# Optimization experiments

Measured on AMD Instinct MI355X. Metric: run time of the kernel, lower is better.

## Reference

```python
import jax, jax.numpy as jnp
import numpy as np

VOCAB = 32000   # config['vocab_size']
D = 512         # embedding dim
H = 512         # config['VarDecoder']['gru']['out_dims']
B = 32          # batch_size = len(batch['var_tok_lens'])
T = 128         # max_len = max(batch['pre_var_tok_lens'])
TOPK = 5        # config['VarDecoder']['topk']
BOS = 1         # tokenizer.bos_token_id
ALPHA = 0.2     # tf.nn.leaky_relu default alpha


def setup_inputs() -> dict:
    key = jax.random.key(0)
    ks = jax.random.split(key, 7)
    s = jnp.float32(0.02)
    return {
        "E": jax.random.normal(ks[0], (VOCAB, D), jnp.float32) * s,      # embedding table
        "Wx": jax.random.normal(ks[1], (D, 3 * H), jnp.float32) * s,     # GRU input kernel [z|r|h]
        "U": jax.random.normal(ks[2], (H, 3 * H), jnp.float32) * s,      # GRU recurrent kernel [z|r|h]
        "b_i": jnp.zeros((3 * H,), jnp.float32),                          # GRU input bias (reset_after)
        "b_r": jnp.zeros((3 * H,), jnp.float32),                          # GRU recurrent bias (reset_after)
        "Wo": jax.random.normal(ks[3], (H, VOCAB), jnp.float32) * s,     # Dense kernel
        "bo": jnp.zeros((VOCAB,), jnp.float32),                           # Dense bias
        "context": jax.random.normal(ks[4], (B, H), jnp.float32),        # initial GRU state
        "rand_idx": jax.random.randint(ks[5], (T, B), 0, TOPK, jnp.int32),  # per-step uniform top-k pick
    }


def reference(E, Wx, U, b_i, b_r, Wo, bo, context, rand_idx):
    def step(carry, ridx):
        tok, h = carry                               # tok: [B] int32, h: [B, H]
        x = jax.nn.leaky_relu(E[tok], ALPHA)         # embedding + leaky_relu  [B, D]
        xg = x @ Wx + b_i                            # [B, 3H]
        hg = h @ U + b_r                             # [B, 3H] (keras reset_after=True)
        xz, xr, xh = jnp.split(xg, 3, axis=-1)
        hz, hr, hh = jnp.split(hg, 3, axis=-1)
        z = jax.nn.sigmoid(xz + hz)
        r = jax.nn.sigmoid(xr + hr)
        cand = jnp.tanh(xh + r * hh)
        h2 = z * h + (1.0 - z) * cand                # keras GRU update
        logits = h2 @ Wo + bo                        # [B, VOCAB]
        _, topk_idx = jax.lax.top_k(logits, TOPK)    # [B, TOPK]
        sel = jnp.take_along_axis(topk_idx, ridx[:, None], axis=1)[:, 0]  # random pick among top-k
        return (sel, h2), logits

    tok0 = jnp.full((B,), BOS, jnp.int32)
    (_, _), logits = jax.lax.scan(step, (tok0, context), rand_idx)
    return jnp.transpose(logits, (1, 0, 2))          # [B, T, VOCAB]
```

## Files before the change

kernel.cpp:

```cpp
#include <hip/hip_runtime.h>
#include <hip/hip_cooperative_groups.h>

namespace cg = cooperative_groups;

#define VOCAB   32000
#define DIM     512
#define HDIM    512
#define BATCH   32
#define TSTEPS  128
#define TOPKN   5
#define BOSTOK  1
#define ALPHA   0.2f
#define G3H     1536

#define NBLK    256
#define NTHR    256
#define GEMMBLK 250
#define CPB     128
#define KH      256
#define H2LD    (KH + 1)

struct alignas(16) SMem {
    float h2h[BATCH][H2LD];
    float sx[DIM];
    float dd[3][64];
    float mbv[4][BATCH][TOPKN];
    int   mbi[4][BATCH][TOPKN];
    float mrgv[4];
    int   mrgi[4];
    int   mrgt[4];
};

__device__ __forceinline__ bool better(float v1, int i1, float v2, int i2) {
    return (v1 > v2) || (v1 == v2 && i1 < i2);
}

__device__ __forceinline__ void ins5(float (&lv)[TOPKN], int (&li)[TOPKN], float v, int i) {
    if (better(v, i, lv[4], li[4])) {
        lv[4] = v; li[4] = i;
#pragma unroll
        for (int q = 4; q > 0; --q) {
            if (better(lv[q], li[q], lv[q - 1], li[q - 1])) {
                float tv = lv[q]; lv[q] = lv[q - 1]; lv[q - 1] = tv;
                int   ti = li[q]; li[q] = li[q - 1]; li[q - 1] = ti;
            }
        }
    }
}

__device__ __forceinline__ float dot256(const float* __restrict__ M, const float* sv,
                                        int c, int kb, float acc) {
    const float* p = M + (size_t)kb * G3H + c;
    float wa[32], wb[32];
#pragma unroll
    for (int u = 0; u < 32; ++u) wa[u] = p[(size_t)u * G3H];
    for (int k0 = 0; k0 < KH; k0 += 64) {
#pragma unroll
        for (int u = 0; u < 32; ++u) wb[u] = p[(size_t)(k0 + 32 + u) * G3H];
#pragma unroll
        for (int u = 0; u < 32; ++u) acc = fmaf(sv[k0 + u], wa[u], acc);
        if (k0 + 64 < KH) {
#pragma unroll
            for (int u = 0; u < 32; ++u) wa[u] = p[(size_t)(k0 + 64 + u) * G3H];
        }
#pragma unroll
        for (int u = 0; u < 32; ++u) acc = fmaf(sv[k0 + 32 + u], wb[u], acc);
    }
    return acc;
}

__device__ __forceinline__ void stage_half(SMem& s, const float* __restrict__ src,
                                           int kb, int tid) {
#pragma unroll
    for (int it = 0; it < 8; ++it) {
        const int i  = tid + it * NTHR;
        const int bb = i >> 6;
        const int k4 = i & 63;
        const float4 v = *(const float4*)(src + (size_t)bb * DIM + kb + k4 * 4);
        float* d = &s.h2h[bb][k4 * 4];
        d[0] = v.x; d[1] = v.y; d[2] = v.z; d[3] = v.w;
    }
}

__device__ __forceinline__ void loadg(float4 (&wv)[8], float (&av)[8][4],
                                      const float* __restrict__ wp, const SMem& s,
                                      int bg, int kb, int k0) {
#pragma unroll
    for (int u = 0; u < 8; ++u) {
        wv[u] = *(const float4*)(wp + (size_t)(kb + k0 + u) * VOCAB);
#pragma unroll
        for (int bi = 0; bi < 4; ++bi)
            av[u][bi] = s.h2h[bg * 4 + bi][k0 + u];
    }
}

__device__ __forceinline__ void fmacg(float (&acc)[4][4], const float4 (&wv)[8],
                                      const float (&av)[8][4]) {
#pragma unroll
    for (int u = 0; u < 8; ++u) {
#pragma unroll
        for (int bi = 0; bi < 4; ++bi) {
            const float a = av[u][bi];
            acc[bi][0] = fmaf(a, wv[u].x, acc[bi][0]);
            acc[bi][1] = fmaf(a, wv[u].y, acc[bi][1]);
            acc[bi][2] = fmaf(a, wv[u].z, acc[bi][2]);
            acc[bi][3] = fmaf(a, wv[u].w, acc[bi][3]);
        }
    }
}

__device__ __forceinline__ void prologue_hg(SMem& s, int j, int tid,
                                            const float* __restrict__ U,
                                            const float* __restrict__ b_r,
                                            const float* __restrict__ hsrc,
                                            float* __restrict__ hg) {
    const int g  = j * 192 + tid;
    const int bb = (tid < 192) ? (g / G3H) : 0;
    const int c  = (tid < 192) ? (g - bb * G3H) : 0;
    float hacc = (tid < 192) ? b_r[c] : 0.f;
    for (int half = 0; half < 2; ++half) {
        const int kb = half * KH;
        __syncthreads();
        stage_half(s, hsrc, kb, tid);
        __syncthreads();
        if (tid < 192) hacc = dot256(U, s.h2h[bb], c, kb, hacc);
    }
    if (tid < 192) hg[g] = hacc;
}

__device__ __forceinline__ void phaseA(SMem& s, int j, int tid, int t,
    const float* __restrict__ U,  const float* __restrict__ b_r,
    const float* __restrict__ Wo, const float* __restrict__ bo,
    const float* __restrict__ hsrc, float* __restrict__ out,
    float* __restrict__ hg, float* __restrict__ pval, int* __restrict__ pidx)
{
    const int w   = tid >> 6;
    const int l   = tid & 63;
    const int bg  = l >> 3;
    const int cg2 = l & 7;
    const int cbase = j * CPB + w * 32 + cg2 * 4;
    const bool gemmer = (j < GEMMBLK);

    const int g     = j * 192 + tid;
    const int hb_bb = (tid < 192) ? (g / G3H) : 0;
    const int hb_c  = (tid < 192) ? (g - hb_bb * G3H) : 0;
    float hacc = (tid < 192) ? b_r[hb_c] : 0.f;

    float acc[4][4] = {};

    for (int half = 0; half < 2; ++half) {
        const int kb = half * KH;
        __syncthreads();
        stage_half(s, hsrc, kb, tid);
        __syncthreads();
        if (gemmer) {
            const float* wp = Wo + cbase;
            float4 wva[8], wvb[8];
            float  ava[8][4], avb[8][4];
            loadg(wva, ava, wp, s, bg, kb, 0);
            for (int k0 = 0; k0 < KH; k0 += 16) {
                loadg(wvb, avb, wp, s, bg, kb, k0 + 8);
                fmacg(acc, wva, ava);
                if (k0 + 16 < KH) loadg(wva, ava, wp, s, bg, kb, k0 + 16);
                fmacg(acc, wvb, avb);
            }
        }
        if (tid < 192) hacc = dot256(U, s.h2h[hb_bb], hb_c, kb, hacc);
    }

    if (tid < 192) hg[g] = hacc;

    if (gemmer) {
        const float4 bov = *(const float4*)(bo + cbase);
#pragma unroll
        for (int bi = 0; bi < 4; ++bi) {
            const int bb = bg * 4 + bi;
            float4 v;
            v.x = acc[bi][0] + bov.x;
            v.y = acc[bi][1] + bov.y;
            v.z = acc[bi][2] + bov.z;
            v.w = acc[bi][3] + bov.w;
            *(float4*)(out + ((size_t)bb * TSTEPS + t) * VOCAB + cbase) = v;

            float lv[TOPKN]; int li[TOPKN];
#pragma unroll
            for (int q = 0; q < TOPKN; ++q) { lv[q] = -INFINITY; li[q] = 0x7fffffff; }
            ins5(lv, li, v.x, cbase + 0);
            ins5(lv, li, v.y, cbase + 1);
            ins5(lv, li, v.z, cbase + 2);
            ins5(lv, li, v.w, cbase + 3);
#pragma unroll
            for (int mask = 1; mask < 8; mask <<= 1) {
                float ov[TOPKN]; int oi[TOPKN];
#pragma unroll
                for (int q = 0; q < TOPKN; ++q) {
                    ov[q] = __shfl_xor(lv[q], mask);
                    oi[q] = __shfl_xor(li[q], mask);
                }
#pragma unroll
                for (int q = 0; q < TOPKN; ++q) ins5(lv, li, ov[q], oi[q]);
            }
            if (cg2 == 0) {
#pragma unroll
                for (int q = 0; q < TOPKN; ++q) { s.mbv[w][bb][q] = lv[q]; s.mbi[w][bb][q] = li[q]; }
            }
        }
    }
    __syncthreads();
    if (gemmer && tid < BATCH) {
        float lv[TOPKN]; int li[TOPKN];
#pragma unroll
        for (int q = 0; q < TOPKN; ++q) { lv[q] = -INFINITY; li[q] = 0x7fffffff; }
#pragma unroll
        for (int w4 = 0; w4 < 4; ++w4)
#pragma unroll
            for (int q = 0; q < TOPKN; ++q)
                ins5(lv, li, s.mbv[w4][tid][q], s.mbi[w4][tid][q]);
        const size_t base = ((size_t)tid * NBLK + j) * TOPKN;
#pragma unroll
        for (int q = 0; q < TOPKN; ++q) { pval[base + q] = lv[q]; pidx[base + q] = li[q]; }
    }
}

__device__ __forceinline__ void phaseB(SMem& s, int j, int tid, int t,
    const float* __restrict__ E,   const float* __restrict__ Wx,
    const float* __restrict__ b_i, const int* __restrict__ rix,
    const float* __restrict__ hg,  const float* __restrict__ pval,
    const int* __restrict__ pidx,  const float* __restrict__ hcur,
    float* __restrict__ hnxt)
{
    const int bat = j >> 3;
    const int jj  = (j & 7) * 64;
    int sel = BOSTOK;
    if (t > 0) {
        float lv[TOPKN]; int li[TOPKN];
        if (tid < GEMMBLK) {
            const size_t base = ((size_t)bat * NBLK + tid) * TOPKN;
#pragma unroll
            for (int q = 0; q < TOPKN; ++q) { lv[q] = pval[base + q]; li[q] = pidx[base + q]; }
        } else {
#pragma unroll
            for (int q = 0; q < TOPKN; ++q) { lv[q] = -INFINITY; li[q] = 0x7fffffff; }
        }
        const int ridx = rix[(t - 1) * BATCH + bat];
        for (int r = 0; r < TOPKN; ++r) {
            float cv = lv[0]; int ci = li[0]; int ct = tid;
#pragma unroll
            for (int mask = 1; mask < 64; mask <<= 1) {
                const float ov = __shfl_xor(cv, mask);
                const int   oi = __shfl_xor(ci, mask);
                const int   ot = __shfl_xor(ct, mask);
                if (better(ov, oi, cv, ci)) { cv = ov; ci = oi; ct = ot; }
            }
            if ((tid & 63) == 0) { s.mrgv[tid >> 6] = cv; s.mrgi[tid >> 6] = ci; s.mrgt[tid >> 6] = ct; }
            __syncthreads();
            float bv = s.mrgv[0]; int bi_ = s.mrgi[0]; int bt = s.mrgt[0];
#pragma unroll
            for (int wq = 1; wq < 4; ++wq)
                if (better(s.mrgv[wq], s.mrgi[wq], bv, bi_)) { bv = s.mrgv[wq]; bi_ = s.mrgi[wq]; bt = s.mrgt[wq]; }
            if (r == ridx) sel = bi_;
            __syncthreads();
            if (tid == bt) {
                lv[0]=lv[1]; li[0]=li[1]; lv[1]=lv[2]; li[1]=li[2];
                lv[2]=lv[3]; li[2]=li[3]; lv[3]=lv[4]; li[3]=li[4];
                lv[4] = -INFINITY; li[4] = 0x7fffffff;
            }
        }
    }
    for (int i = tid; i < DIM; i += NTHR) {
        const float e = E[(size_t)sel * DIM + i];
        s.sx[i] = e > 0.f ? e : ALPHA * e;
    }
    __syncthreads();
    if (tid < 192) {
        const int o = tid & 63, part = tid >> 6;
        const int c = jj + o + part * HDIM;
        float a = b_i[c];
        a = dot256(Wx, s.sx, c, 0, a);
        a = dot256(Wx, s.sx + KH, c, KH, a);
        s.dd[part][o] = a;
    }
    __syncthreads();
    if (tid < 64) {
        const int c = jj + tid;
        const float xz = s.dd[0][tid], xr = s.dd[1][tid], xh = s.dd[2][tid];
        const float* hgb = hg + (size_t)bat * G3H;
        const float hz = hgb[c], hr = hgb[c + HDIM], hh = hgb[c + 2 * HDIM];
        const float z    = 1.f / (1.f + expf(-(xz + hz)));
        const float r    = 1.f / (1.f + expf(-(xr + hr)));
        const float cand = tanhf(xh + r * hh);
        const float hold = hcur[bat * HDIM + c];
        hnxt[bat * HDIM + c] = z * hold + (1.f - z) * cand;
    }
}

static __global__ void __launch_bounds__(NTHR, 1)
gru_coop(const float* __restrict__ E,  const float* __restrict__ Wx,
         const float* __restrict__ U,  const float* __restrict__ b_i,
         const float* __restrict__ b_r,const float* __restrict__ Wo,
         const float* __restrict__ bo, const float* __restrict__ ctx,
         const int* __restrict__ rix,  float* __restrict__ out,
         float* __restrict__ hbuf,     float* __restrict__ hg,
         float* __restrict__ pval,     int* __restrict__ pidx)
{
    cg::grid_group grid = cg::this_grid();
    const int j = blockIdx.x, tid = threadIdx.x;
    __shared__ SMem s;
    {
        const int g1 = j * NTHR + tid;
        if (g1 < (BATCH * HDIM) / 4) ((float4*)hbuf)[g1] = ((const float4*)ctx)[g1];
    }
    prologue_hg(s, j, tid, U, b_r, ctx, hg);
    grid.sync();
    for (int t = 0; t < TSTEPS; ++t) {
        const int p = t & 1;
        const float* hcur = hbuf + p * (BATCH * HDIM);
        float*       hnxt = hbuf + (p ^ 1) * (BATCH * HDIM);
        phaseB(s, j, tid, t, E, Wx, b_i, rix, hg, pval, pidx, hcur, hnxt);
        grid.sync();
        phaseA(s, j, tid, t, U, b_r, Wo, bo, hnxt, out, hg, pval, pidx);
        grid.sync();
    }
}

static __global__ void __launch_bounds__(NTHR, 1)
k_prologue(const float* __restrict__ U, const float* __restrict__ b_r,
           const float* __restrict__ ctx, float* __restrict__ hbuf,
           float* __restrict__ hg)
{
    __shared__ SMem s;
    const int j = blockIdx.x, tid = threadIdx.x;
    const int g1 = j * NTHR + tid;
    if (g1 < (BATCH * HDIM) / 4) ((float4*)hbuf)[g1] = ((const float4*)ctx)[g1];
    prologue_hg(s, j, tid, U, b_r, ctx, hg);
}

static __global__ void __launch_bounds__(NTHR, 1)
k_phaseB(int t, const float* __restrict__ E, const float* __restrict__ Wx,
         const float* __restrict__ b_i, const int* __restrict__ rix,
         const float* __restrict__ hg, const float* __restrict__ pval,
         const int* __restrict__ pidx, float* __restrict__ hbuf)
{
    __shared__ SMem s;
    const int p = t & 1;
    phaseB(s, blockIdx.x, threadIdx.x, t, E, Wx, b_i, rix, hg, pval, pidx,
           hbuf + p * (BATCH * HDIM), hbuf + (p ^ 1) * (BATCH * HDIM));
}

static __global__ void __launch_bounds__(NTHR, 1)
k_phaseA(int t, const float* __restrict__ U, const float* __restrict__ b_r,
         const float* __restrict__ Wo, const float* __restrict__ bo,
         const float* __restrict__ hbuf, float* __restrict__ out,
         float* __restrict__ hg, float* __restrict__ pval, int* __restrict__ pidx)
{
    __shared__ SMem s;
    const int p = t & 1;
    phaseA(s, blockIdx.x, threadIdx.x, t, U, b_r, Wo, bo,
           hbuf + (p ^ 1) * (BATCH * HDIM), out, hg, pval, pidx);
}

extern "C" void kernel_launch(void* const* d_in, const int* in_sizes, int n_in,
                              void* d_out, int out_size, void* d_ws, size_t ws_size,
                              hipStream_t stream) {
    (void)in_sizes; (void)n_in; (void)out_size; (void)ws_size;
    const float* E   = (const float*)d_in[0];
    const float* Wx  = (const float*)d_in[1];
    const float* U   = (const float*)d_in[2];
    const float* b_i = (const float*)d_in[3];
    const float* b_r = (const float*)d_in[4];
    const float* Wo  = (const float*)d_in[5];
    const float* bo  = (const float*)d_in[6];
    const float* ctx = (const float*)d_in[7];
    const int*   rix = (const int*)d_in[8];
    float* out = (float*)d_out;

    float* ws   = (float*)d_ws;
    float* hbuf = ws;
    float* hg   = ws + 32768;
    float* pval = ws + 81920;
    int*   pidx = (int*)(ws + 122880);

    int dev = 0;
    (void)hipGetDevice(&dev);
    int coopAttr = 0, numCU = 0, maxBlk = 0;
    (void)hipDeviceGetAttribute(&coopAttr, hipDeviceAttributeCooperativeLaunch, dev);
    (void)hipDeviceGetAttribute(&numCU, hipDeviceAttributeMultiprocessorCount, dev);
    (void)hipOccupancyMaxActiveBlocksPerMultiprocessor(&maxBlk, gru_coop, NTHR, 0);

    bool coop_done = false;
    if (coopAttr && maxBlk >= 1 && (long)maxBlk * numCU >= NBLK) {
        void* args[] = {&E, &Wx, &U, &b_i, &b_r, &Wo, &bo, &ctx, &rix,
                        &out, &hbuf, &hg, &pval, &pidx};
        hipError_t e = hipLaunchCooperativeKernel(gru_coop, dim3(NBLK), dim3(NTHR),
                                                  args, 0u, stream);
        if (e == hipSuccess) coop_done = true;
        else (void)hipGetLastError();
    }
    if (!coop_done) {
        k_prologue<<<dim3(NBLK), dim3(NTHR), 0, stream>>>(U, b_r, ctx, hbuf, hg);
        for (int t = 0; t < TSTEPS; ++t) {
            k_phaseB<<<dim3(NBLK), dim3(NTHR), 0, stream>>>(t, E, Wx, b_i, rix,
                                                            hg, pval, pidx, hbuf);
            k_phaseA<<<dim3(NBLK), dim3(NTHR), 0, stream>>>(t, U, b_r, Wo, bo,
                                                            hbuf, out, hg, pval, pidx);
        }
    }
}
```

Measured before the change: 10.09 ms.

## Add MFMA bf16 cooperative GRU decode path with fp32 top-k candidate rescoring

Adds a new cooperative kernel that pre-transposes and packs Wo into bf16 MFMA fragments and computes the vocab logits with 16x16x32 bf16 MFMA instead of fp32 FMA loops. Because the bf16 logits can reorder the top-k, it merges the 8 best candidates per batch row and recomputes them in fp32 from a transposed Wo copy before choosing the token. The step is restructured into three grid-synced phases, and U and Wx are transposed to make the gate dot products contiguous. This needs roughly 105 MB of workspace and adds one grid sync per step. The logits written to the output carry bf16-level error.

```diff
diff --git a/kernel.cpp b/kernel.cpp
--- a/kernel.cpp
+++ b/kernel.cpp
@@ -9,6 +9,7 @@
 #define BATCH   32
 #define TSTEPS  128
 #define TOPKN   5
+#define CAND    8
 #define BOSTOK  1
 #define ALPHA   0.2f
 #define G3H     1536
@@ -17,6 +18,350 @@
 #define NTHR    256
 #define GEMMBLK 250
 #define CPB     128
+
+__device__ __forceinline__ bool better(float v1, int i1, float v2, int i2) {
+    return (v1 > v2) || (v1 == v2 && i1 < i2);
+}
+
+__device__ __forceinline__ void ins5(float (&lv)[TOPKN], int (&li)[TOPKN], float v, int i) {
+    if (better(v, i, lv[4], li[4])) {
+        lv[4] = v; li[4] = i;
+#pragma unroll
+        for (int q = 4; q > 0; --q) {
+            if (better(lv[q], li[q], lv[q - 1], li[q - 1])) {
+                float tv = lv[q]; lv[q] = lv[q - 1]; lv[q - 1] = tv;
+                int   ti = li[q]; li[q] = li[q - 1]; li[q - 1] = ti;
+            }
+        }
+    }
+}
+
+__device__ __forceinline__ unsigned f2bf(float f) {
+    unsigned u = __float_as_uint(f);
+    return (u + 0x7FFFu + ((u >> 16) & 1u)) >> 16;
+}
+
+
+typedef __bf16 bf16x8 __attribute__((ext_vector_type(8)));
+typedef float  f32x4  __attribute__((ext_vector_type(4)));
+
+struct SMemN_run {
+    unsigned afrag[2][16][64][4];
+    float pwv[4][BATCH][TOPKN];
+    int   pwi[4][BATCH][TOPKN];
+    float xgs[BATCH][6];
+    int   sel[BATCH];
+    float mrgv[4]; int mrgi[4]; int mrgt[4];
+};
+struct SMemN_pro { float tile[64][129]; };
+union  SMemN { SMemN_pro pro; SMemN_run run; };
+
+__device__ __forceinline__ void hg_compute(int j, int tid, const float* __restrict__ h2,
+                                           const float* __restrict__ UT,
+                                           const float* __restrict__ b_r,
+                                           float* __restrict__ hg) {
+    if (tid < 192) {
+        const int g  = j * 192 + tid;
+        const int bb = g / G3H;
+        const int c  = g - bb * G3H;
+        const float4* hp = (const float4*)(h2 + bb * HDIM);
+        const float4* up = (const float4*)(UT + (size_t)c * HDIM);
+        float a = b_r[c];
+#pragma unroll 4
+        for (int i = 0; i < HDIM / 4; ++i) {
+            float4 h = hp[i], u = up[i];
+            a = fmaf(h.x, u.x, fmaf(h.y, u.y, fmaf(h.z, u.z, fmaf(h.w, u.w, a))));
+        }
+        hg[g] = a;
+    }
+}
+
+__device__ void prologue_new(SMemN& s, int j, int tid,
+    const float* __restrict__ Wo, const float* __restrict__ U,
+    const float* __restrict__ Wx, const float* __restrict__ ctx,
+    unsigned* __restrict__ WoPk, float* __restrict__ WoT,
+    float* __restrict__ UT, float* __restrict__ WxT, float* __restrict__ h2)
+{
+    if (tid < 64) {
+        const int bb = tid >> 1, c = 2 * j + (tid & 1);
+        h2[bb * HDIM + c] = ctx[bb * HDIM + c];
+    }
+    for (int i = tid; i < 6 * DIM; i += NTHR) {
+        const int rr = i >> 9, k = i & 511;
+        const int gc = (rr >> 1) * HDIM + 2 * j + (rr & 1);
+        UT[(size_t)gc * DIM + k]  = U[(size_t)k * G3H + gc];
+        WxT[(size_t)gc * DIM + k] = Wx[(size_t)k * G3H + gc];
+    }
+    if (j < GEMMBLK) {
+        for (int chunk = 0; chunk < 8; ++chunk) {
+            const int k0 = chunk * 64;
+            __syncthreads();
+#pragma unroll
+            for (int it = 0; it < 8; ++it) {
+                const int idx = tid + it * NTHR;
+                const int kk = idx >> 5, c4 = (idx & 31) << 2;
+                const float4 v = *(const float4*)(Wo + (size_t)(k0 + kk) * VOCAB + j * CPB + c4);
+                s.pro.tile[kk][c4] = v.x; s.pro.tile[kk][c4 + 1] = v.y;
+                s.pro.tile[kk][c4 + 2] = v.z; s.pro.tile[kk][c4 + 3] = v.w;
+            }
+            __syncthreads();
+            {
+                const int kh = tid >> 7, c = tid & 127;
+                float* dst = WoT + ((size_t)j * CPB + c) * DIM + k0 + kh * 32;
+#pragma unroll
+                for (int kk = 0; kk < 32; ++kk) dst[kk] = s.pro.tile[kh * 32 + kk][c];
+            }
+#pragma unroll
+            for (int uu = 0; uu < 4; ++uu) {
+                const int u = tid + uu * NTHR;
+                const int kss = u >> 9, nt = (u >> 6) & 7, ll = u & 63;
+                const int kb = kss * 32 + ((ll >> 4) << 3);
+                const int c  = nt * 16 + (ll & 15);
+                unsigned d[4];
+#pragma unroll
+                for (int e2 = 0; e2 < 4; ++e2) {
+                    const unsigned lo = f2bf(s.pro.tile[kb + 2 * e2][c]);
+                    const unsigned hi = f2bf(s.pro.tile[kb + 2 * e2 + 1][c]);
+                    d[e2] = lo | (hi << 16);
+                }
+                const int ksg = chunk * 2 + kss;
+                uint4* dst = (uint4*)WoPk + ((((size_t)j * 16 + ksg) * 8 + nt) * 64 + ll);
+                *dst = *(const uint4*)d;
+            }
+        }
+    }
+}
+
+__device__ __forceinline__ void phaseA_new(SMemN& s, int j, int tid, int t,
+    const unsigned* __restrict__ WoPk, const float* __restrict__ bo,
+    const float* __restrict__ h2, const float* __restrict__ UT,
+    const float* __restrict__ b_r, float* __restrict__ out,
+    float* __restrict__ hg, float* __restrict__ pval, int* __restrict__ pidx)
+{
+#pragma unroll
+    for (int q = 0; q < 8; ++q) {
+        const int f = tid + q * NTHR;
+        const int m = f >> 10, ks = (f >> 6) & 15, lf = f & 63;
+        const int row = (lf & 15) + 16 * m;
+        const int kb  = ks * 32 + ((lf >> 4) << 3);
+        const float4* hp = (const float4*)(h2 + row * DIM + kb);
+        const float4 a0 = hp[0], a1 = hp[1];
+        unsigned* d = &s.run.afrag[m][ks][lf][0];
+        d[0] = f2bf(a0.x) | (f2bf(a0.y) << 16);
+        d[1] = f2bf(a0.z) | (f2bf(a0.w) << 16);
+        d[2] = f2bf(a1.x) | (f2bf(a1.y) << 16);
+        d[3] = f2bf(a1.z) | (f2bf(a1.w) << 16);
+    }
+    __syncthreads();
+    const int w = tid >> 6, l = tid & 63;
+    if (j < GEMMBLK) {
+        f32x4 acc[2][2];
+        acc[0][0] = {0.f, 0.f, 0.f, 0.f}; acc[0][1] = {0.f, 0.f, 0.f, 0.f};
+        acc[1][0] = {0.f, 0.f, 0.f, 0.f}; acc[1][1] = {0.f, 0.f, 0.f, 0.f};
+        const uint4* wpk = (const uint4*)WoPk;
+#pragma unroll 4
+        for (int ks = 0; ks < 16; ++ks) {
+            const uint4 b0 = wpk[(((size_t)j * 16 + ks) * 8 + 2 * w) * 64 + l];
+            const uint4 b1 = wpk[(((size_t)j * 16 + ks) * 8 + 2 * w + 1) * 64 + l];
+            const uint4 a0 = *(const uint4*)&s.run.afrag[0][ks][l][0];
+            const uint4 a1 = *(const uint4*)&s.run.afrag[1][ks][l][0];
+            const bf16x8 A0 = __builtin_bit_cast(bf16x8, a0);
+            const bf16x8 A1 = __builtin_bit_cast(bf16x8, a1);
+            const bf16x8 B0 = __builtin_bit_cast(bf16x8, b0);
+            const bf16x8 B1 = __builtin_bit_cast(bf16x8, b1);
+            acc[0][0] = __builtin_amdgcn_mfma_f32_16x16x32_bf16(A0, B0, acc[0][0], 0, 0, 0);
+            acc[0][1] = __builtin_amdgcn_mfma_f32_16x16x32_bf16(A0, B1, acc[0][1], 0, 0, 0);
+            acc[1][0] = __builtin_amdgcn_mfma_f32_16x16x32_bf16(A1, B0, acc[1][0], 0, 0, 0);
+            acc[1][1] = __builtin_amdgcn_mfma_f32_16x16x32_bf16(A1, B1, acc[1][1], 0, 0, 0);
+        }
+        const int c0 = j * CPB + (2 * w) * 16 + (l & 15);
+        const int c1 = j * CPB + (2 * w + 1) * 16 + (l & 15);
+        const float bo0 = bo[c0], bo1 = bo[c1];
+#pragma unroll
+        for (int m = 0; m < 2; ++m) {
+#pragma unroll
+            for (int r = 0; r < 4; ++r) {
+                const int b = 16 * m + ((l >> 4) << 2) + r;
+                const float v0 = acc[m][0][r] + bo0;
+                const float v1 = acc[m][1][r] + bo1;
+                __builtin_nontemporal_store(v0, out + ((size_t)b * TSTEPS + t) * VOCAB + c0);
+                __builtin_nontemporal_store(v1, out + ((size_t)b * TSTEPS + t) * VOCAB + c1);
+                float lv[TOPKN]; int li[TOPKN];
+#pragma unroll
+                for (int q = 0; q < TOPKN; ++q) { lv[q] = -INFINITY; li[q] = 0x7fffffff; }
+                ins5(lv, li, v0, c0);
+                ins5(lv, li, v1, c1);
+#pragma unroll
+                for (int mask = 1; mask < 16; mask <<= 1) {
+                    float ov[TOPKN]; int oi[TOPKN];
+#pragma unroll
+                    for (int q = 0; q < TOPKN; ++q) {
+                        ov[q] = __shfl_xor(lv[q], mask);
+                        oi[q] = __shfl_xor(li[q], mask);
+                    }
+#pragma unroll
+                    for (int q = 0; q < TOPKN; ++q) ins5(lv, li, ov[q], oi[q]);
+                }
+                if ((l & 15) == 0) {
+#pragma unroll
+                    for (int q = 0; q < TOPKN; ++q) { s.run.pwv[w][b][q] = lv[q]; s.run.pwi[w][b][q] = li[q]; }
+                }
+            }
+        }
+    }
+    hg_compute(j, tid, h2, UT, b_r, hg);
+    __syncthreads();
+    if (j < GEMMBLK && tid < BATCH) {
+        float lv[TOPKN]; int li[TOPKN];
+#pragma unroll
+        for (int q = 0; q < TOPKN; ++q) { lv[q] = -INFINITY; li[q] = 0x7fffffff; }
+#pragma unroll
+        for (int w4 = 0; w4 < 4; ++w4)
+#pragma unroll
+            for (int q = 0; q < TOPKN; ++q) ins5(lv, li, s.run.pwv[w4][tid][q], s.run.pwi[w4][tid][q]);
+        const size_t base = ((size_t)tid * NBLK + j) * TOPKN;
+#pragma unroll
+        for (int q = 0; q < TOPKN; ++q) { pval[base + q] = lv[q]; pidx[base + q] = li[q]; }
+    }
+}
+
+__device__ __forceinline__ void phaseB_new(SMemN& s, int j, int tid,
+    const float* __restrict__ pval, const int* __restrict__ pidx,
+    const float* __restrict__ h2, const float* __restrict__ WoT,
+    const float* __restrict__ bo, float* __restrict__ exV, int* __restrict__ exI)
+{
+    const int bat = j >> 3;
+    float lv[TOPKN]; int li[TOPKN];
+    if (tid < GEMMBLK) {
+        const size_t base = ((size_t)bat * NBLK + tid) * TOPKN;
+#pragma unroll
+        for (int q = 0; q < TOPKN; ++q) { lv[q] = pval[base + q]; li[q] = pidx[base + q]; }
+    } else {
+#pragma unroll
+        for (int q = 0; q < TOPKN; ++q) { lv[q] = -INFINITY; li[q] = 0x7fffffff; }
+    }
+    int cnd = 0;
+    const int myrank = j & 7;
+    for (int r = 0; r < CAND; ++r) {
+        float cv = lv[0]; int ci = li[0]; int ct = tid;
+#pragma unroll
+        for (int mask = 1; mask < 64; mask <<= 1) {
+            const float ov = __shfl_xor(cv, mask);
+            const int   oi = __shfl_xor(ci, mask);
+            const int   ot = __shfl_xor(ct, mask);
+            if (better(ov, oi, cv, ci)) { cv = ov; ci = oi; ct = ot; }
+        }
+        if ((tid & 63) == 0) { s.run.mrgv[tid >> 6] = cv; s.run.mrgi[tid >> 6] = ci; s.run.mrgt[tid >> 6] = ct; }
+        __syncthreads();
+        float bv = s.run.mrgv[0]; int bi_ = s.run.mrgi[0]; int bt = s.run.mrgt[0];
+#pragma unroll
+        for (int wq = 1; wq < 4; ++wq)
+            if (better(s.run.mrgv[wq], s.run.mrgi[wq], bv, bi_)) { bv = s.run.mrgv[wq]; bi_ = s.run.mrgi[wq]; bt = s.run.mrgt[wq]; }
+        if (r == myrank) cnd = bi_;
+        __syncthreads();
+        if (tid == bt) {
+            lv[0] = lv[1]; li[0] = li[1]; lv[1] = lv[2]; li[1] = li[2];
+            lv[2] = lv[3]; li[2] = li[3]; lv[3] = lv[4]; li[3] = li[4];
+            lv[4] = -INFINITY; li[4] = 0x7fffffff;
+        }
+    }
+    if (tid < 64) {
+        const float4* wp = (const float4*)(WoT + (size_t)cnd * DIM);
+        const float4* hp = (const float4*)(h2 + bat * HDIM);
+        float a = 0.f;
+#pragma unroll
+        for (int ii = 0; ii < 2; ++ii) {
+            const int i = tid + ii * 64;
+            const float4 wv = wp[i], hv = hp[i];
+            a = fmaf(hv.x, wv.x, fmaf(hv.y, wv.y, fmaf(hv.z, wv.z, fmaf(hv.w, wv.w, a))));
+        }
+#pragma unroll
+        for (int mask = 1; mask < 64; mask <<= 1) a += __shfl_xor(a, mask);
+        if (tid == 0) { exV[bat * CAND + myrank] = a + bo[cnd]; exI[bat * CAND + myrank] = cnd; }
+    }
+}
+
+__device__ __forceinline__ void phaseC_new(SMemN& s, int j, int tid, int t,
+    const float* __restrict__ E, const float* __restrict__ WxT,
+    const float* __restrict__ b_i, const int* __restrict__ rix,
+    const float* __restrict__ hg, const float* __restrict__ exV,
+    const int* __restrict__ exI, float* __restrict__ h2)
+{
+    if (tid < BATCH) {
+        int sl = BOSTOK;
+        if (t > 0) {
+            float lv[TOPKN]; int li[TOPKN];
+#pragma unroll
+            for (int q = 0; q < TOPKN; ++q) { lv[q] = -INFINITY; li[q] = 0x7fffffff; }
+#pragma unroll
+            for (int r = 0; r < CAND; ++r) ins5(lv, li, exV[tid * CAND + r], exI[tid * CAND + r]);
+            sl = li[rix[(t - 1) * BATCH + tid]];
+        }
+        s.run.sel[tid] = sl;
+    }
+    __syncthreads();
+    if (tid < 192) {
+        const int bb = tid & 31, p = tid >> 5;
+        const int gc = (p >> 1) * HDIM + 2 * j + (p & 1);
+        const float4* er = (const float4*)(E + (size_t)s.run.sel[bb] * DIM);
+        const float4* wx = (const float4*)(WxT + (size_t)gc * DIM);
+        float a = b_i[gc];
+#pragma unroll 2
+        for (int i = 0; i < DIM / 4; ++i) {
+            const float4 e4 = er[i], w4 = wx[i];
+            const float x0 = e4.x > 0.f ? e4.x : ALPHA * e4.x;
+            const float x1 = e4.y > 0.f ? e4.y : ALPHA * e4.y;
+            const float x2 = e4.z > 0.f ? e4.z : ALPHA * e4.z;
+            const float x3 = e4.w > 0.f ? e4.w : ALPHA * e4.w;
+            a = fmaf(x0, w4.x, fmaf(x1, w4.y, fmaf(x2, w4.z, fmaf(x3, w4.w, a))));
+        }
+        s.run.xgs[bb][p] = a;
+    }
+    __syncthreads();
+    if (tid < 64) {
+        const int bb = tid >> 1, q = tid & 1;
+        const int hc = 2 * j + q;
+        const float xz = s.run.xgs[bb][q], xr = s.run.xgs[bb][2 + q], xh = s.run.xgs[bb][4 + q];
+        const float* hgb = hg + (size_t)bb * G3H;
+        const float hz = hgb[hc], hr = hgb[HDIM + hc], hh = hgb[2 * HDIM + hc];
+        const float z   = 1.f / (1.f + expf(-(xz + hz)));
+        const float r   = 1.f / (1.f + expf(-(xr + hr)));
+        const float cd  = tanhf(xh + r * hh);
+        const float hold = h2[bb * HDIM + hc];
+        h2[bb * HDIM + hc] = z * hold + (1.f - z) * cd;
+    }
+}
+
+static __global__ void __launch_bounds__(NTHR, 1)
+gru_mfma(const float* __restrict__ E,  const float* __restrict__ Wx,
+         const float* __restrict__ U,  const float* __restrict__ b_i,
+         const float* __restrict__ b_r, const float* __restrict__ Wo,
+         const float* __restrict__ bo, const float* __restrict__ ctx,
+         const int* __restrict__ rix,  float* __restrict__ out,
+         unsigned* __restrict__ WoPk,  float* __restrict__ WoT,
+         float* __restrict__ UT,       float* __restrict__ WxT,
+         float* __restrict__ h2,       float* __restrict__ hg,
+         float* __restrict__ pval,     int* __restrict__ pidx,
+         float* __restrict__ exV,      int* __restrict__ exI)
+{
+    cg::grid_group grid = cg::this_grid();
+    const int j = blockIdx.x, tid = threadIdx.x;
+    __shared__ SMemN s;
+    prologue_new(s, j, tid, Wo, U, Wx, ctx, WoPk, WoT, UT, WxT, h2);
+    grid.sync();
+    hg_compute(j, tid, h2, UT, b_r, hg);
+    grid.sync();
+    for (int t = 0; t < TSTEPS; ++t) {
+        if (t > 0) phaseB_new(s, j, tid, pval, pidx, h2, WoT, bo, exV, exI);
+        grid.sync();
+        phaseC_new(s, j, tid, t, E, WxT, b_i, rix, hg, exV, exI, h2);
+        grid.sync();
+        phaseA_new(s, j, tid, t, WoPk, bo, h2, UT, b_r, out, hg, pval, pidx);
+        grid.sync();
+    }
+}
+
+
 #define KH      256
 #define H2LD    (KH + 1)
 
@@ -31,23 +376,6 @@
     int   mrgt[4];
 };
 
-__device__ __forceinline__ bool better(float v1, int i1, float v2, int i2) {
-    return (v1 > v2) || (v1 == v2 && i1 < i2);
-}
-
-__device__ __forceinline__ void ins5(float (&lv)[TOPKN], int (&li)[TOPKN], float v, int i) {
-    if (better(v, i, lv[4], li[4])) {
-        lv[4] = v; li[4] = i;
-#pragma unroll
-        for (int q = 4; q > 0; --q) {
-            if (better(lv[q], li[q], lv[q - 1], li[q - 1])) {
-                float tv = lv[q]; lv[q] = lv[q - 1]; lv[q - 1] = tv;
-                int   ti = li[q]; li[q] = li[q - 1]; li[q - 1] = ti;
-            }
-        }
-    }
-}
-
 __device__ __forceinline__ float dot256(const float* __restrict__ M, const float* sv,
                                         int c, int kb, float acc) {
     const float* p = M + (size_t)kb * G3H + c;
@@ -89,8 +417,7 @@
     for (int u = 0; u < 8; ++u) {
         wv[u] = *(const float4*)(wp + (size_t)(kb + k0 + u) * VOCAB);
 #pragma unroll
-        for (int bi = 0; bi < 4; ++bi)
-            av[u][bi] = s.h2h[bg * 4 + bi][k0 + u];
+        for (int bi = 0; bi < 4; ++bi) av[u][bi] = s.h2h[bg * 4 + bi][k0 + u];
     }
 }
 
@@ -214,8 +541,7 @@
 #pragma unroll
         for (int w4 = 0; w4 < 4; ++w4)
 #pragma unroll
-            for (int q = 0; q < TOPKN; ++q)
-                ins5(lv, li, s.mbv[w4][tid][q], s.mbi[w4][tid][q]);
+            for (int q = 0; q < TOPKN; ++q) ins5(lv, li, s.mbv[w4][tid][q], s.mbi[w4][tid][q]);
         const size_t base = ((size_t)tid * NBLK + j) * TOPKN;
 #pragma unroll
         for (int q = 0; q < TOPKN; ++q) { pval[base + q] = lv[q]; pidx[base + q] = li[q]; }
@@ -362,7 +688,7 @@
 extern "C" void kernel_launch(void* const* d_in, const int* in_sizes, int n_in,
                               void* d_out, int out_size, void* d_ws, size_t ws_size,
                               hipStream_t stream) {
-    (void)in_sizes; (void)n_in; (void)out_size; (void)ws_size;
+    (void)in_sizes; (void)n_in; (void)out_size;
     const float* E   = (const float*)d_in[0];
     const float* Wx  = (const float*)d_in[1];
     const float* U   = (const float*)d_in[2];
@@ -374,35 +700,74 @@
     const int*   rix = (const int*)d_in[8];
     float* out = (float*)d_out;
 
-    float* ws   = (float*)d_ws;
-    float* hbuf = ws;
-    float* hg   = ws + 32768;
-    float* pval = ws + 81920;
-    int*   pidx = (int*)(ws + 122880);
-
     int dev = 0;
     (void)hipGetDevice(&dev);
-    int coopAttr = 0, numCU = 0, maxBlk = 0;
+    int coopAttr = 0, numCU = 0;
     (void)hipDeviceGetAttribute(&coopAttr, hipDeviceAttributeCooperativeLaunch, dev);
     (void)hipDeviceGetAttribute(&numCU, hipDeviceAttributeMultiprocessorCount, dev);
-    (void)hipOccupancyMaxActiveBlocksPerMultiprocessor(&maxBlk, gru_coop, NTHR, 0);
-
-    bool coop_done = false;
-    if (coopAttr && maxBlk >= 1 && (long)maxBlk * numCU >= NBLK) {
-        void* args[] = {&E, &Wx, &U, &b_i, &b_r, &Wo, &bo, &ctx, &rix,
-                        &out, &hbuf, &hg, &pval, &pidx};
-        hipError_t e = hipLaunchCooperativeKernel(gru_coop, dim3(NBLK), dim3(NTHR),
-                                                  args, 0u, stream);
-        if (e == hipSuccess) coop_done = true;
-        else (void)hipGetLastError();
-    }
-    if (!coop_done) {
-        k_prologue<<<dim3(NBLK), dim3(NTHR), 0, stream>>>(U, b_r, ctx, hbuf, hg);
-        for (int t = 0; t < TSTEPS; ++t) {
-            k_phaseB<<<dim3(NBLK), dim3(NTHR), 0, stream>>>(t, E, Wx, b_i, rix,
-                                                            hg, pval, pidx, hbuf);
-            k_phaseA<<<dim3(NBLK), dim3(NTHR), 0, stream>>>(t, U, b_r, Wo, bo,
-                                                            hbuf, out, hg, pval, pidx);
-        }
-    }
-}
+
+    const size_t oWoPk = 0;
+    const size_t oWoT  = 32768000;
+    const size_t oUT   = 98304000;
+    const size_t oWxT  = 101449728;
+    const size_t oh2   = 104595456;
+    const size_t ohg   = 104660992;
+    const size_t opval = 104857600;
+    const size_t opidx = 105021440;
+    const size_t oexV  = 105185280;
+    const size_t oexI  = 105186304;
+    const size_t need  = 105187328;
+
+    bool launched = false;
+    if (coopAttr && ws_size >= need) {
+        int maxBlk = 0;
+        (void)hipOccupancyMaxActiveBlocksPerMultiprocessor(&maxBlk, gru_mfma, NTHR, 0);
+        if (maxBlk >= 1 && (long)maxBlk * numCU >= NBLK) {
+            char* w = (char*)d_ws;
+            unsigned* WoPk = (unsigned*)(w + oWoPk);
+            float* WoT  = (float*)(w + oWoT);
+            float* UT   = (float*)(w + oUT);
+            float* WxT  = (float*)(w + oWxT);
+            float* h2   = (float*)(w + oh2);
+            float* hg   = (float*)(w + ohg);
+            float* pval = (float*)(w + opval);
+            int*   pidx = (int*)(w + opidx);
+            float* exV  = (float*)(w + oexV);
+            int*   exI  = (int*)(w + oexI);
+            void* args[] = {&E, &Wx, &U, &b_i, &b_r, &Wo, &bo, &ctx, &rix, &out,
+                            &WoPk, &WoT, &UT, &WxT, &h2, &hg, &pval, &pidx, &exV, &exI};
+            if (hipLaunchCooperativeKernel(gru_mfma, dim3(NBLK), dim3(NTHR),
+                                           args, 0u, stream) == hipSuccess) launched = true;
+            else (void)hipGetLastError();
+        }
+    }
+
+    if (!launched) {
+        float* ws   = (float*)d_ws;
+        float* hbuf = ws;
+        float* hg   = ws + 32768;
+        float* pval = ws + 81920;
+        int*   pidx = (int*)(ws + 122880);
+        bool coop_done = false;
+        if (coopAttr) {
+            int maxBlk = 0;
+            (void)hipOccupancyMaxActiveBlocksPerMultiprocessor(&maxBlk, gru_coop, NTHR, 0);
+            if (maxBlk >= 1 && (long)maxBlk * numCU >= NBLK) {
+                void* args[] = {&E, &Wx, &U, &b_i, &b_r, &Wo, &bo, &ctx, &rix,
+                                &out, &hbuf, &hg, &pval, &pidx};
+                if (hipLaunchCooperativeKernel(gru_coop, dim3(NBLK), dim3(NTHR),
+                                               args, 0u, stream) == hipSuccess) coop_done = true;
+                else (void)hipGetLastError();
+            }
+        }
+        if (!coop_done) {
+            k_prologue<<<dim3(NBLK), dim3(NTHR), 0, stream>>>(U, b_r, ctx, hbuf, hg);
+            for (int t = 0; t < TSTEPS; ++t) {
+                k_phaseB<<<dim3(NBLK), dim3(NTHR), 0, stream>>>(t, E, Wx, b_i, rix,
+                                                                hg, pval, pidx, hbuf);
+                k_phaseA<<<dim3(NBLK), dim3(NTHR), 0, stream>>>(t, U, b_r, Wo, bo,
+                                                                hbuf, out, hg, pval, pidx);
+            }
+        }
+    }
+}
```

After: 24.10 ms. 139% more time.
